# Kernel tuning notes

Measured on AMD Instinct MI355X. Metric: run time of the kernel, lower is better.

The kernel has to match this reference:

```python
import jax, jax.numpy as jnp
import numpy as np

NUM_GROUPS = 14
GROUP_IN = 9
SHARED_H = 16
SHARED_OUT = 4
SALE_DIM = 1
FINAL_H = 128
ACTION_DIM = 15


def setup_inputs() -> dict:
    key = jax.random.key(0)
    ks = jax.random.split(key, 10)
    B = 262144
    features_2 = jax.random.normal(ks[0], (B, NUM_GROUPS * GROUP_IN), dtype=jnp.float32)
    sale_predictions = jax.random.normal(ks[1], (B, SALE_DIM), dtype=jnp.float32)
    # shared block params (one block, shared across all 14 groups)
    W1 = jax.random.normal(ks[2], (GROUP_IN, SHARED_H), dtype=jnp.float32) / np.sqrt(GROUP_IN)
    b1 = jnp.zeros((SHARED_H,), dtype=jnp.float32)
    W2 = jax.random.normal(ks[3], (SHARED_H, SHARED_OUT), dtype=jnp.float32) / np.sqrt(SHARED_H)
    b2 = jnp.zeros((SHARED_OUT,), dtype=jnp.float32)
    # final block params
    fin_in = SHARED_OUT * NUM_GROUPS + SALE_DIM  # 57
    W3 = jax.random.normal(ks[4], (fin_in, FINAL_H), dtype=jnp.float32) / np.sqrt(fin_in)
    b3 = jnp.zeros((FINAL_H,), dtype=jnp.float32)
    W4 = jax.random.normal(ks[5], (FINAL_H, ACTION_DIM * 2), dtype=jnp.float32) / np.sqrt(FINAL_H)
    b4 = jnp.zeros((ACTION_DIM * 2,), dtype=jnp.float32)
    return {"features_2": features_2, "sale_predictions": sale_predictions,
            "W1": W1, "b1": b1, "W2": W2, "b2": b2,
            "W3": W3, "b3": b3, "W4": W4, "b4": b4}


def reference(features_2, sale_predictions, W1, b1, W2, b2, W3, b3, W4, b4):
    B = features_2.shape[0]
    # [B, 14, 9]: all 14 groups through the SAME shared block, batched as one GEMM
    g = features_2.reshape(B, NUM_GROUPS, GROUP_IN)
    h = jax.nn.relu(jnp.einsum('bgi,ih->bgh', g, W1) + b1)          # [B,14,16]
    s = jax.nn.relu(jnp.einsum('bgh,ho->bgo', h, W2) + b2)          # [B,14,4]
    shared_outputs = s.reshape(B, NUM_GROUPS * SHARED_OUT)          # [B,56]
    combined = jnp.concatenate([shared_outputs, sale_predictions], axis=1)  # [B,57]
    z = jax.nn.relu(combined @ W3 + b3)                             # [B,128]
    out = z @ W4 + b4                                               # [B,30]
    action_mean, action_log_std = jnp.split(out, 2, axis=1)
    action_mean = jnp.tanh(action_mean)
    action_std = jnp.exp(action_log_std)
    return (action_mean, action_std)
```

## Files before the change

### kernel.cpp

```cpp
#include <hip/hip_runtime.h>


typedef float f4v  __attribute__((ext_vector_type(4)));
typedef short s8v  __attribute__((ext_vector_type(8)));
typedef _Float16 h2v __attribute__((ext_vector_type(2)));
typedef unsigned u2v __attribute__((ext_vector_type(2)));
typedef unsigned u4v __attribute__((ext_vector_type(4)));

constexpr int NG = 14, GI = 9, FH = 128, AD = 15;

__device__ __forceinline__ unsigned short f2bf(float f) {
    unsigned u = __builtin_bit_cast(unsigned, f);
    return (unsigned short)((u + 0x7fffu + ((u >> 16) & 1u)) >> 16);
}
__device__ __forceinline__ float bf2f(unsigned short h) {
    return __builtin_bit_cast(float, (unsigned)h << 16);
}
__device__ __forceinline__ f4v load4u(const float* p) {
    f4v v; __builtin_memcpy(&v, p, 16); return v;
}
__device__ __forceinline__ unsigned pkh(float a, float b) {
    return __builtin_bit_cast(unsigned, __builtin_amdgcn_cvt_pkrtz(a, b));
}
__device__ __forceinline__ unsigned pkbf(float a, float b) {
    unsigned r;
    asm("v_cvt_pk_bf16_f32 %0, %1, %2" : "=v"(r) : "v"(a), "v"(b));
    return r;
}

__global__ void pack_kernel(const float* __restrict__ W3,
                            const float* __restrict__ W4,
                            const float* __restrict__ W1,
                            const float* __restrict__ b1,
                            const float* __restrict__ W2,
                            unsigned short* __restrict__ pk) {
    unsigned short* W3h = pk;
    unsigned short* W3l = pk + 8192;
    unsigned short* W4h = pk + 16384;
    unsigned short* W4l = pk + 20480;
    unsigned* pk32 = (unsigned*)pk;
    int t = blockIdx.x * 256 + threadIdx.x;
    if (t < 8192) {
        int j = t & 7, l = (t >> 3) & 63, nt = (t >> 9) & 7, kt = t >> 12;
        int k = kt * 32 + (l >> 4) * 8 + j, n = nt * 16 + (l & 15);
        float v = (k < 57) ? W3[k * FH + n] : 0.f;
        unsigned short h = f2bf(v);
        W3h[t] = h;
        W3l[t] = f2bf(v - bf2f(h));
    }
    if (t < 4096) {
        int j = t & 7, l = (t >> 3) & 63, nt = (t >> 9) & 1, kt = t >> 10;
        int k = kt * 32 + (l >> 4) * 8 + j, n = nt * 16 + (l & 15);
        float v = (n < 30) ? W4[k * 30 + n] : 0.f;
        unsigned short h = f2bf(v);
        W4h[t] = h;
        W4l[t] = f2bf(v - bf2f(h));
    }
    if (t < 72) {
        int i = t >> 3, j2 = t & 7;
        pk32[12288 + t] = pkh(W1[i * 16 + 2 * j2], W1[i * 16 + 2 * j2 + 1]);
    }
    if (t < 8)
        pk32[12360 + t] = pkh(b1[2 * t], b1[2 * t + 1]);
    if (t < 32) {
        int j2 = t >> 2, o = t & 3;
        pk32[12368 + t] = pkh(W2[(2 * j2) * 4 + o], W2[(2 * j2 + 1) * 4 + o]);
    }
}

__global__ __launch_bounds__(256, 4) void actor_fused(
    const float* __restrict__ x,
    const float* __restrict__ sale,
    const float* __restrict__ b2,
    const float* __restrict__ b3,
    const float* __restrict__ b4,
    const unsigned short* __restrict__ pk,
    float* __restrict__ om, float* __restrict__ os)
{
    __shared__ unsigned short xz[8192];
    __shared__ unsigned short sh[4096];

    const int tid  = threadIdx.x;
    const int wv   = __builtin_amdgcn_readfirstlane(tid >> 6);
    const int lane = tid & 63;
    const int row0 = blockIdx.x * 64;

    {
        const float* xs = x + (size_t)(row0 + 16 * wv) * (NG * GI);
        unsigned* xw = (unsigned*)(xz + 16 * wv * 126);
        #pragma unroll
        for (int j = 0; j < 8; ++j) {
            int ci = j * 64 + lane;
            if (j < 7 || ci < 504) {
                f4v v = load4u(xs + 4 * ci);
                xw[2 * ci]     = pkh(v[0], v[1]);
                xw[2 * ci + 1] = pkh(v[2], v[3]);
            }
        }
    }
    if (lane < 16) {
        int r = 16 * wv + lane;
        float sv = sale[row0 + r];
        int byt = (r * 128 + 112) ^ ((r & 7) << 4);
        *(unsigned short*)((char*)sh + byt) = f2bf(sv);
        #pragma unroll
        for (int kk = 57; kk < 64; ++kk) {
            int bb = (r * 128 + kk * 2) ^ ((r & 7) << 4);
            *(unsigned short*)((char*)sh + bb) = 0;
        }
    }

    const int r1 = 16 * wv + (lane & 15);
    const int q  = lane >> 4;
    const h2v* w1p = (const h2v*)(pk + 24576);
    const h2v* b1p = (const h2v*)(pk + 24720);
    const h2v* w2p = (const h2v*)(pk + 24736);
    const _Float16* xhp = (const _Float16*)xz;

    auto do_group = [&](int gg) {
        const int hb = r1 * 126 + gg * 9;
        h2v h0 = b1p[0], h1 = b1p[1], h2 = b1p[2], h3 = b1p[3],
            h4 = b1p[4], h5 = b1p[5], h6 = b1p[6], h7 = b1p[7];
        #pragma unroll
        for (int i = 0; i < 9; ++i) {
            _Float16 xs1 = xhp[hb + i];
            h2v xb = (h2v){xs1, xs1};
            const h2v* wr = w1p + i * 8;
            h0 += xb * wr[0]; h1 += xb * wr[1];
            h2 += xb * wr[2]; h3 += xb * wr[3];
            h4 += xb * wr[4]; h5 += xb * wr[5];
            h6 += xb * wr[6]; h7 += xb * wr[7];
        }
        const h2v zz = (h2v)(_Float16)0;
        h0 = __builtin_elementwise_max(h0, zz);
        h1 = __builtin_elementwise_max(h1, zz);
        h2 = __builtin_elementwise_max(h2, zz);
        h3 = __builtin_elementwise_max(h3, zz);
        h4 = __builtin_elementwise_max(h4, zz);
        h5 = __builtin_elementwise_max(h5, zz);
        h6 = __builtin_elementwise_max(h6, zz);
        h7 = __builtin_elementwise_max(h7, zz);
        float sv4[4];
        #pragma unroll
        for (int o = 0; o < 4; ++o) {
            h2v a2 = zz;
            a2 += h0 * w2p[0 * 4 + o];
            a2 += h1 * w2p[1 * 4 + o];
            a2 += h2 * w2p[2 * 4 + o];
            a2 += h3 * w2p[3 * 4 + o];
            a2 += h4 * w2p[4 * 4 + o];
            a2 += h5 * w2p[5 * 4 + o];
            a2 += h6 * w2p[6 * 4 + o];
            a2 += h7 * w2p[7 * 4 + o];
            float s = (float)a2[0] + (float)a2[1] + b2[o];
            sv4[o] = fmaxf(s, 0.f);
        }
        unsigned p01 = pkbf(sv4[0], sv4[1]);
        unsigned p23 = pkbf(sv4[2], sv4[3]);
        int byt = (r1 * 128 + gg * 8) ^ ((r1 & 7) << 4);
        *(u2v*)((char*)sh + byt) = (u2v){p01, p23};
    };
    do_group(q); do_group(q + 4); do_group(q + 8);
    if (q < 2) do_group(q + 12);

    __syncthreads();

    const s8v* W3hv = (const s8v*)pk;
    const s8v* W3lv = (const s8v*)(pk + 8192);
    s8v bh[2][2], bl[2][2];
    #pragma unroll
    for (int kt = 0; kt < 2; ++kt)
        #pragma unroll
        for (int ntl = 0; ntl < 2; ++ntl) {
            int nt = 2 * wv + ntl;
            bh[kt][ntl] = W3hv[(kt * 8 + nt) * 64 + lane];
            bl[kt][ntl] = W3lv[(kt * 8 + nt) * 64 + lane];
        }
    f4v acc[4][2];
    #pragma unroll
    for (int ntl = 0; ntl < 2; ++ntl) {
        float bv = b3[32 * wv + ntl * 16 + (lane & 15)];
        #pragma unroll
        for (int mt = 0; mt < 4; ++mt) acc[mt][ntl] = (f4v){bv, bv, bv, bv};
    }
    #pragma unroll
    for (int kt = 0; kt < 2; ++kt) {
        s8v ah[4];
        #pragma unroll
        for (int mt = 0; mt < 4; ++mt) {
            int rr = mt * 16 + (lane & 15);
            int byt = (rr * 128 + kt * 64 + (lane >> 4) * 16) ^ ((rr & 7) << 4);
            ah[mt] = *(const s8v*)((char*)sh + byt);
        }
        #pragma unroll
        for (int mt = 0; mt < 4; ++mt)
            #pragma unroll
            for (int ntl = 0; ntl < 2; ++ntl) {
                acc[mt][ntl] = __builtin_amdgcn_mfma_f32_16x16x32_bf16(ah[mt], bh[kt][ntl], acc[mt][ntl], 0, 0, 0);
                acc[mt][ntl] = __builtin_amdgcn_mfma_f32_16x16x32_bf16(ah[mt], bl[kt][ntl], acc[mt][ntl], 0, 0, 0);
            }
    }
    #pragma unroll
    for (int mt = 0; mt < 4; ++mt)
        #pragma unroll
        for (int ntl = 0; ntl < 2; ++ntl) {
            int kk  = ntl * 16 + (lane & 15);
            int tau = (kk & 4) ? 4 + (kk >> 3) : (kk >> 3);
            int eidx = mt * 2048 + wv * 512 + tau * 64 + (kk & 3) * 16
                     + ((lane >> 4) << 2);
            float v0 = fmaxf(acc[mt][ntl][0], 0.f);
            float v1 = fmaxf(acc[mt][ntl][1], 0.f);
            float v2 = fmaxf(acc[mt][ntl][2], 0.f);
            float v3 = fmaxf(acc[mt][ntl][3], 0.f);
            *(u2v*)(xz + eidx) = (u2v){pkbf(v0, v1), pkbf(v2, v3)};
        }

    __syncthreads();

    const s8v* W4hv = (const s8v*)(pk + 16384);
    const s8v* W4lv = (const s8v*)(pk + 20480);
    const int mq   = __builtin_amdgcn_readfirstlane(wv >> 1);
    const int nq   = __builtin_amdgcn_readfirstlane(wv & 1);
    const int ocol = nq * 16 + (lane & 15);
    const float b4i = (ocol < 30) ? b4[ocol] : 0.f;

    s8v wh[4], wl[4];
    #pragma unroll
    for (int kt = 0; kt < 4; ++kt) {
        wh[kt] = W4hv[(kt * 2 + nq) * 64 + lane];
        wl[kt] = W4lv[(kt * 2 + nq) * 64 + lane];
    }
    unsigned base = (unsigned)(size_t)&xz[0] + (unsigned)(2 * mq) * 4096u
                  + (unsigned)(lane * 8);
    u2v f0[4][2], f1[4][2];
    #pragma unroll
    for (int c = 0; c < 4; ++c) {
        unsigned a0 = base + c * 1024;
        unsigned a1 = a0 + 4096;
        asm volatile("ds_read_b64_tr_b16 %0, %1" : "=v"(f0[c][0]) : "v"(a0));
        asm volatile("ds_read_b64_tr_b16 %0, %1 offset:512" : "=v"(f0[c][1]) : "v"(a0));
        asm volatile("ds_read_b64_tr_b16 %0, %1" : "=v"(f1[c][0]) : "v"(a1));
        asm volatile("ds_read_b64_tr_b16 %0, %1 offset:512" : "=v"(f1[c][1]) : "v"(a1));
    }
    asm volatile("s_waitcnt lgkmcnt(0)" ::: "memory");
    __builtin_amdgcn_sched_barrier(0);

    f4v oa0 = (f4v){b4i, b4i, b4i, b4i};
    f4v oa1 = oa0;
    #pragma unroll
    for (int kt = 0; kt < 4; ++kt) {
        s8v z0 = __builtin_bit_cast(s8v,
            (u4v){f0[kt][0][0], f0[kt][0][1], f0[kt][1][0], f0[kt][1][1]});
        s8v z1 = __builtin_bit_cast(s8v,
            (u4v){f1[kt][0][0], f1[kt][0][1], f1[kt][1][0], f1[kt][1][1]});
        oa0 = __builtin_amdgcn_mfma_f32_16x16x32_bf16(z0, wh[kt], oa0, 0, 0, 0);
        oa0 = __builtin_amdgcn_mfma_f32_16x16x32_bf16(z0, wl[kt], oa0, 0, 0, 0);
        oa1 = __builtin_amdgcn_mfma_f32_16x16x32_bf16(z1, wh[kt], oa1, 0, 0, 0);
        oa1 = __builtin_amdgcn_mfma_f32_16x16x32_bf16(z1, wl[kt], oa1, 0, 0, 0);
    }
    #pragma unroll
    for (int mi = 0; mi < 2; ++mi) {
        f4v oa = mi ? oa1 : oa0;
        #pragma unroll
        for (int i = 0; i < 4; ++i) {
            int grow = row0 + mq * 32 + mi * 16 + (lane >> 4) * 4 + i;
            float v = oa[i];
            if (ocol < AD) {
                float tc = fminf(fmaxf(v, -20.f), 20.f);
                float e = __expf(2.f * tc);
                om[(size_t)grow * AD + ocol] = (e - 1.f) / (e + 1.f);
            } else if (ocol < 2 * AD) {
                os[(size_t)grow * AD + (ocol - AD)] = __expf(v);
            }
        }
    }
}

extern "C" void kernel_launch(void* const* d_in, const int* in_sizes, int n_in,
                              void* d_out, int out_size, void* d_ws, size_t ws_size,
                              hipStream_t stream) {
    const float* x    = (const float*)d_in[0];
    const float* sale = (const float*)d_in[1];
    const float* W1   = (const float*)d_in[2];
    const float* b1   = (const float*)d_in[3];
    const float* W2   = (const float*)d_in[4];
    const float* b2   = (const float*)d_in[5];
    const float* W3   = (const float*)d_in[6];
    const float* b3   = (const float*)d_in[7];
    const float* W4   = (const float*)d_in[8];
    const float* b4   = (const float*)d_in[9];

    int B = in_sizes[1];
    float* om = (float*)d_out;
    float* os = om + (size_t)B * AD;
    unsigned short* pk = (unsigned short*)d_ws;

    pack_kernel<<<32, 256, 0, stream>>>(W3, W4, W1, b1, W2, pk);
    actor_fused<<<B / 64, 256, 0, stream>>>(x, sale, b2, b3, b4, pk, om, os);
}
```

Measured before the change: 50.01 us.

## Compute shared per-group MLP with f16 MFMA instead of packed-half VALU

Replaces the per-lane packed-half FMA evaluation of the shared 9->16->4 block with two 16x16x32 f16 MFMAs per group. The weights are pre-packed into MFMA fragment layout, with K split across lane quarters and masked. This moves the group MLP off VALU onto the matrix unit and accumulates in fp32 instead of fp16, but wastes most of the MFMA K dimension and has only one lane quarter write results. It also merges the x staging stores into 64-bit LDS writes.

```diff
diff --git a/kernel.cpp b/kernel.cpp
--- a/kernel.cpp
+++ b/kernel.cpp
@@ -3,7 +3,7 @@
 
 typedef float f4v  __attribute__((ext_vector_type(4)));
 typedef short s8v  __attribute__((ext_vector_type(8)));
-typedef _Float16 h2v __attribute__((ext_vector_type(2)));
+typedef _Float16 h8v __attribute__((ext_vector_type(8)));
 typedef unsigned u2v __attribute__((ext_vector_type(2)));
 typedef unsigned u4v __attribute__((ext_vector_type(4)));
 
@@ -31,14 +31,12 @@
 __global__ void pack_kernel(const float* __restrict__ W3,
                             const float* __restrict__ W4,
                             const float* __restrict__ W1,
-                            const float* __restrict__ b1,
                             const float* __restrict__ W2,
                             unsigned short* __restrict__ pk) {
     unsigned short* W3h = pk;
     unsigned short* W3l = pk + 8192;
     unsigned short* W4h = pk + 16384;
     unsigned short* W4l = pk + 20480;
-    unsigned* pk32 = (unsigned*)pk;
     int t = blockIdx.x * 256 + threadIdx.x;
     if (t < 8192) {
         int j = t & 7, l = (t >> 3) & 63, nt = (t >> 9) & 7, kt = t >> 12;
@@ -56,21 +54,22 @@
         W4h[t] = h;
         W4l[t] = f2bf(v - bf2f(h));
     }
-    if (t < 72) {
-        int i = t >> 3, j2 = t & 7;
-        pk32[12288 + t] = pkh(W1[i * 16 + 2 * j2], W1[i * 16 + 2 * j2 + 1]);
-    }
-    if (t < 8)
-        pk32[12360 + t] = pkh(b1[2 * t], b1[2 * t + 1]);
-    if (t < 32) {
-        int j2 = t >> 2, o = t & 3;
-        pk32[12368 + t] = pkh(W2[(2 * j2) * 4 + o], W2[(2 * j2 + 1) * 4 + o]);
+    if (t < 512) {
+        int l = t >> 3, j = t & 7;
+        int p = l >> 4, m = l & 15;
+        int k = (j < 4) ? (p * 4 + j) : (16 + p * 4 + (j - 4));
+        float v1 = (k < GI) ? W1[k * 16 + m] : 0.f;
+        float v2 = (k < 16 && m < 4) ? W2[k * 4 + m] : 0.f;
+        _Float16 h1 = (_Float16)v1, h2 = (_Float16)v2;
+        pk[24576 + t] = __builtin_bit_cast(unsigned short, h1);
+        pk[25088 + t] = __builtin_bit_cast(unsigned short, h2);
     }
 }
 
 __global__ __launch_bounds__(256, 4) void actor_fused(
     const float* __restrict__ x,
     const float* __restrict__ sale,
+    const float* __restrict__ b1,
     const float* __restrict__ b2,
     const float* __restrict__ b3,
     const float* __restrict__ b4,
@@ -84,6 +83,8 @@
     const int wv   = __builtin_amdgcn_readfirstlane(tid >> 6);
     const int lane = tid & 63;
     const int row0 = blockIdx.x * 64;
+    const int p    = lane >> 4;
+    const int col  = lane & 15;
 
     {
         const float* xs = x + (size_t)(row0 + 16 * wv) * (NG * GI);
@@ -93,8 +94,7 @@
             int ci = j * 64 + lane;
             if (j < 7 || ci < 504) {
                 f4v v = load4u(xs + 4 * ci);
-                xw[2 * ci]     = pkh(v[0], v[1]);
-                xw[2 * ci + 1] = pkh(v[2], v[3]);
+                *(u2v*)(xw + 2 * ci) = (u2v){pkh(v[0], v[1]), pkh(v[2], v[3])};
             }
         }
     }
@@ -110,58 +110,37 @@
         }
     }
 
-    const int r1 = 16 * wv + (lane & 15);
-    const int q  = lane >> 4;
-    const h2v* w1p = (const h2v*)(pk + 24576);
-    const h2v* b1p = (const h2v*)(pk + 24720);
-    const h2v* w2p = (const h2v*)(pk + 24736);
-    const _Float16* xhp = (const _Float16*)xz;
-
-    auto do_group = [&](int gg) {
-        const int hb = r1 * 126 + gg * 9;
-        h2v h0 = b1p[0], h1 = b1p[1], h2 = b1p[2], h3 = b1p[3],
-            h4 = b1p[4], h5 = b1p[5], h6 = b1p[6], h7 = b1p[7];
-        #pragma unroll
-        for (int i = 0; i < 9; ++i) {
-            _Float16 xs1 = xhp[hb + i];
-            h2v xb = (h2v){xs1, xs1};
-            const h2v* wr = w1p + i * 8;
-            h0 += xb * wr[0]; h1 += xb * wr[1];
-            h2 += xb * wr[2]; h3 += xb * wr[3];
-            h4 += xb * wr[4]; h5 += xb * wr[5];
-            h6 += xb * wr[6]; h7 += xb * wr[7];
-        }
-        const h2v zz = (h2v)(_Float16)0;
-        h0 = __builtin_elementwise_max(h0, zz);
-        h1 = __builtin_elementwise_max(h1, zz);
-        h2 = __builtin_elementwise_max(h2, zz);
-        h3 = __builtin_elementwise_max(h3, zz);
-        h4 = __builtin_elementwise_max(h4, zz);
-        h5 = __builtin_elementwise_max(h5, zz);
-        h6 = __builtin_elementwise_max(h6, zz);
-        h7 = __builtin_elementwise_max(h7, zz);
-        float sv4[4];
-        #pragma unroll
-        for (int o = 0; o < 4; ++o) {
-            h2v a2 = zz;
-            a2 += h0 * w2p[0 * 4 + o];
-            a2 += h1 * w2p[1 * 4 + o];
-            a2 += h2 * w2p[2 * 4 + o];
-            a2 += h3 * w2p[3 * 4 + o];
-            a2 += h4 * w2p[4 * 4 + o];
-            a2 += h5 * w2p[5 * 4 + o];
-            a2 += h6 * w2p[6 * 4 + o];
-            a2 += h7 * w2p[7 * 4 + o];
-            float s = (float)a2[0] + (float)a2[1] + b2[o];
-            sv4[o] = fmaxf(s, 0.f);
-        }
-        unsigned p01 = pkbf(sv4[0], sv4[1]);
-        unsigned p23 = pkbf(sv4[2], sv4[3]);
-        int byt = (r1 * 128 + gg * 8) ^ ((r1 & 7) << 4);
-        *(u2v*)((char*)sh + byt) = (u2v){p01, p23};
-    };
-    do_group(q); do_group(q + 4); do_group(q + 8);
-    if (q < 2) do_group(q + 12);
+    const int r1 = 16 * wv + col;
+    const h8v w1t = __builtin_bit_cast(h8v, *(const s8v*)(pk + 24576 + lane * 8));
+    const h8v w2t = __builtin_bit_cast(h8v, *(const s8v*)(pk + 25088 + lane * 8));
+    const f4v b1f = load4u(b1 + p * 4);
+    const f4v b2f = load4u(b2);
+    const unsigned m0 = (p < 2) ? 0xFFFFFFFFu : (p == 2 ? 0x0000FFFFu : 0u);
+    const unsigned m1 = (p < 2) ? 0xFFFFFFFFu : 0u;
+    const unsigned short* xbase = xz + (r1 * 126 + p * 4);
+    const int sbase = r1 * 128;
+    const int ssw   = (r1 & 7) << 4;
+
+    #pragma unroll
+    for (int g = 0; g < NG; ++g) {
+        unsigned l0 = xbase[g * 9 + 0], l1 = xbase[g * 9 + 1];
+        unsigned l2 = xbase[g * 9 + 2], l3 = xbase[g * 9 + 3];
+        unsigned u0 = (l0 | (l1 << 16)) & m0;
+        unsigned u1 = (l2 | (l3 << 16)) & m1;
+        h8v xb = __builtin_bit_cast(h8v, (u4v){u0, u1, 0u, 0u});
+        f4v ha = __builtin_amdgcn_mfma_f32_16x16x32_f16(w1t, xb, b1f, 0, 0, 0);
+        float h0 = fmaxf(ha[0], 0.f), h1 = fmaxf(ha[1], 0.f);
+        float h2 = fmaxf(ha[2], 0.f), h3 = fmaxf(ha[3], 0.f);
+        h8v hb = __builtin_bit_cast(h8v, (u4v){pkh(h0, h1), pkh(h2, h3), 0u, 0u});
+        f4v sa = __builtin_amdgcn_mfma_f32_16x16x32_f16(w2t, hb, b2f, 0, 0, 0);
+        float s0 = fmaxf(sa[0], 0.f), s1 = fmaxf(sa[1], 0.f);
+        float s2 = fmaxf(sa[2], 0.f), s3 = fmaxf(sa[3], 0.f);
+        unsigned q0 = pkbf(s0, s1), q1 = pkbf(s2, s3);
+        if (p == 0) {
+            int byt = (sbase + g * 8) ^ ssw;
+            *(u2v*)((char*)sh + byt) = (u2v){q0, q1};
+        }
+    }
 
     __syncthreads();
 
@@ -179,7 +158,7 @@
     f4v acc[4][2];
     #pragma unroll
     for (int ntl = 0; ntl < 2; ++ntl) {
-        float bv = b3[32 * wv + ntl * 16 + (lane & 15)];
+        float bv = b3[32 * wv + ntl * 16 + col];
         #pragma unroll
         for (int mt = 0; mt < 4; ++mt) acc[mt][ntl] = (f4v){bv, bv, bv, bv};
     }
@@ -188,8 +167,8 @@
         s8v ah[4];
         #pragma unroll
         for (int mt = 0; mt < 4; ++mt) {
-            int rr = mt * 16 + (lane & 15);
-            int byt = (rr * 128 + kt * 64 + (lane >> 4) * 16) ^ ((rr & 7) << 4);
+            int rr = mt * 16 + col;
+            int byt = (rr * 128 + kt * 64 + p * 16) ^ ((rr & 7) << 4);
             ah[mt] = *(const s8v*)((char*)sh + byt);
         }
         #pragma unroll
@@ -204,10 +183,9 @@
     for (int mt = 0; mt < 4; ++mt)
         #pragma unroll
         for (int ntl = 0; ntl < 2; ++ntl) {
-            int kk  = ntl * 16 + (lane & 15);
+            int kk  = ntl * 16 + col;
             int tau = (kk & 4) ? 4 + (kk >> 3) : (kk >> 3);
-            int eidx = mt * 2048 + wv * 512 + tau * 64 + (kk & 3) * 16
-                     + ((lane >> 4) << 2);
+            int eidx = mt * 2048 + wv * 512 + tau * 64 + (kk & 3) * 16 + (p << 2);
             float v0 = fmaxf(acc[mt][ntl][0], 0.f);
             float v1 = fmaxf(acc[mt][ntl][1], 0.f);
             float v2 = fmaxf(acc[mt][ntl][2], 0.f);
@@ -221,7 +199,7 @@
     const s8v* W4lv = (const s8v*)(pk + 20480);
     const int mq   = __builtin_amdgcn_readfirstlane(wv >> 1);
     const int nq   = __builtin_amdgcn_readfirstlane(wv & 1);
-    const int ocol = nq * 16 + (lane & 15);
+    const int ocol = nq * 16 + col;
     const float b4i = (ocol < 30) ? b4[ocol] : 0.f;
 
     s8v wh[4], wl[4];
@@ -263,7 +241,7 @@
         f4v oa = mi ? oa1 : oa0;
         #pragma unroll
         for (int i = 0; i < 4; ++i) {
-            int grow = row0 + mq * 32 + mi * 16 + (lane >> 4) * 4 + i;
+            int grow = row0 + mq * 32 + mi * 16 + p * 4 + i;
             float v = oa[i];
             if (ocol < AD) {
                 float tc = fminf(fmaxf(v, -20.f), 20.f);
@@ -295,6 +273,7 @@
     float* os = om + (size_t)B * AD;
     unsigned short* pk = (unsigned short*)d_ws;
 
-    pack_kernel<<<32, 256, 0, stream>>>(W3, W4, W1, b1, W2, pk);
-    actor_fused<<<B / 64, 256, 0, stream>>>(x, sale, b2, b3, b4, pk, om, os);
-}
+    pack_kernel<<<32, 256, 0, stream>>>(W3, W4, W1, W2, pk);
+    actor_fused<<<B / 64, 256, 0, stream>>>(x, sale, b1, b2, b3, b4,
+                                            pk, om, os);
+}
```

New measurement: 50.22 us. No clear change (+0.4%).
